# Performance work log

Measured on AMD Instinct MI355X. Metric: run time of the kernel, lower is better.

The kernel has to match this reference:

```python
import jax, jax.numpy as jnp
import numpy as np

N_HEADS = 16
WINDOW = 128
EPS = 1e-6
NEG_INF = -1e30  # effectively -inf after softmax in fp32


def setup_inputs() -> dict:
    key = jax.random.key(0)
    ks = jax.random.split(key, 5)
    B, T, D = 2, 2048, 1024
    scale = 1.0 / np.sqrt(D)
    return {
        "x": jax.random.normal(ks[0], (B, T, D), dtype=jnp.float32),
        "Wq": jax.random.normal(ks[1], (D, D), dtype=jnp.float32) * scale,
        "Wk": jax.random.normal(ks[2], (D, D), dtype=jnp.float32) * scale,
        "Wv": jax.random.normal(ks[3], (D, D), dtype=jnp.float32) * scale,
        "Wo": jax.random.normal(ks[4], (D, D), dtype=jnp.float32) * scale,
    }


def _l2norm(t):
    # torch F.normalize: t / max(||t||, eps)
    n = jnp.sqrt(jnp.sum(t * t, axis=-1, keepdims=True))
    return t / jnp.maximum(n, EPS)


def reference(x, Wq, Wk, Wv, Wo):
    B, T, D = x.shape
    H, hd = N_HEADS, D // N_HEADS
    # projections (torch Linear: x @ W.T), split heads -> [B, H, T, hd]
    def proj(W):
        return jnp.einsum('btd,ed->bte', x, W).reshape(B, T, H, hd).transpose(0, 2, 1, 3)
    q = _l2norm(proj(Wq))
    k = _l2norm(proj(Wk))
    v = proj(Wv)
    # scores [B, H, T, T] (no 1/sqrt(d) scale in the source)
    attn = jnp.einsum('bhqd,bhkd->bhqk', q, k)
    pos = jnp.arange(T)
    rel = pos[None, :] - pos[:, None]            # rel[i, j] = j - i
    mask = (rel < 0) | (rel >= WINDOW)           # allowed: 0 <= j-i < window
    base = jnp.linspace(0.0, 1.0, H, dtype=x.dtype)
    slopes = jnp.power(jnp.asarray(2.0, x.dtype), -(8.0 * base))  # [H]
    alibi = -jnp.abs(rel).astype(x.dtype)[None, :, :] * slopes[:, None, None]  # [H,T,T]
    bias = jnp.where(mask[None, :, :], jnp.asarray(NEG_INF, x.dtype), alibi)
    attn = jax.nn.softmax(attn + bias[None], axis=-1)
    out = jnp.einsum('bhqk,bhkd->bhqd', attn, v)
    out = out.transpose(0, 2, 1, 3).reshape(B, T, D)
    return jnp.einsum('btd,ed->bte', out, Wo)
```

## Files before the change

### kernel.cpp

```cpp
#include <hip/hip_runtime.h>
#include <hip/hip_bf16.h>

#define T_SEQ   2048
#define BATCH   2
#define DMODEL  1024
#define NHEADS  16
#define HDIM    64
#define WINDOW  128

typedef __attribute__((ext_vector_type(8))) short bf16x8;
typedef __attribute__((ext_vector_type(4))) float f32x4;

__device__ inline void gld_lds16(const __hip_bfloat16* g, __hip_bfloat16* l) {
    __builtin_amdgcn_global_load_lds(
        (const __attribute__((address_space(1))) unsigned int*)g,
        (__attribute__((address_space(3))) unsigned int*)l, 16, 0, 0);
}

__global__ __launch_bounds__(256) void cvt_kernel(
    const float* __restrict__ x,  const float* __restrict__ Wq,
    const float* __restrict__ Wk, const float* __restrict__ Wv,
    const float* __restrict__ Wo,
    __hip_bfloat16* __restrict__ xb, __hip_bfloat16* __restrict__ Wb)
{
    const int lid = blockIdx.x;
    const float* src;
    __hip_bfloat16* dst;
    int blk;
    if (lid < 2048) { src = x; dst = xb; blk = lid; }
    else {
        int slot = (lid - 2048) >> 9;
        blk = (lid - 2048) & 511;
        src = (slot == 0) ? Wq : (slot == 1) ? Wk : (slot == 2) ? Wv : Wo;
        dst = Wb + (size_t)slot * 1024 * 1024;
    }
    int i = (blk * 256 + threadIdx.x) * 8;
    float4 a = *(const float4*)(src + i);
    float4 b = *(const float4*)(src + i + 4);
    __hip_bfloat16 pk[8] = {
        __float2bfloat16(a.x), __float2bfloat16(a.y),
        __float2bfloat16(a.z), __float2bfloat16(a.w),
        __float2bfloat16(b.x), __float2bfloat16(b.y),
        __float2bfloat16(b.z), __float2bfloat16(b.w)};
    *(uint4*)(dst + i) = *(uint4*)pk;
}

__global__ __launch_bounds__(256) void gemm_qkv(
    const __hip_bfloat16* __restrict__ A,
    const __hip_bfloat16* __restrict__ W0,
    const __hip_bfloat16* __restrict__ W1,
    const __hip_bfloat16* __restrict__ W2,
    __hip_bfloat16* __restrict__ C0,
    __hip_bfloat16* __restrict__ C1,
    __hip_bfloat16* __restrict__ C2,
    int M, int N, int K)
{
    const int lid   = blockIdx.x + 8 * blockIdx.y + 256 * blockIdx.z;
    const int xcd   = lid & 7;
    const int s     = lid >> 3;
    const int m_loc = s & 7;
    const int rest  = s >> 3;
    const int n_loc = rest & 3;
    const int z     = rest >> 2;

    const __hip_bfloat16* W = (z == 0) ? W0 : (z == 1 ? W1 : W2);
    __hip_bfloat16* C = (z == 0) ? C0 : (z == 1 ? C1 : C2);

    const int m0 = ((xcd & 3) * 8 + m_loc) * 128;
    const int n0 = ((xcd >> 2) * 4 + n_loc) * 128;

    __shared__ __hip_bfloat16 As[128 * 64];
    __shared__ __hip_bfloat16 Bs[128 * 64];

    const int t    = threadIdx.x;
    const int lane = t & 63;
    const int wv   = t >> 6;

    const int drow = lane >> 3;
    const int sl   = lane & 7;

    const int wm   = (wv >> 1) * 64;
    const int wn   = (wv & 1) * 64;
    const int lrow = lane & 15;
    const int quad = lane >> 4;

    f32x4 acc[4][4];
#pragma unroll
    for (int i = 0; i < 4; i++)
#pragma unroll
        for (int j = 0; j < 4; j++)
            acc[i][j] = (f32x4){0.f, 0.f, 0.f, 0.f};

    for (int k0 = 0; k0 < K; k0 += 64) {
#pragma unroll
        for (int inst = 0; inst < 4; inst++) {
            int r0 = wv * 32 + inst * 8;
            int r  = r0 + drow;
            int gcx = (sl - r) & 7;
            gld_lds16(A + (size_t)(m0 + r) * K + k0 + gcx * 8, &As[r0 * 64]);
            gld_lds16(W + (size_t)(n0 + r) * K + k0 + gcx * 8, &Bs[r0 * 64]);
        }
        __syncthreads();

#pragma unroll
        for (int kk = 0; kk < 2; kk++) {
            bf16x8 af[4], bfv[4];
#pragma unroll
            for (int mi = 0; mi < 4; mi++) {
                int r = wm + mi * 16 + lrow;
                af[mi] = *(const bf16x8*)&As[r * 64 + ((kk * 4 + quad + r) & 7) * 8];
            }
#pragma unroll
            for (int ni = 0; ni < 4; ni++) {
                int r = wn + ni * 16 + lrow;
                bfv[ni] = *(const bf16x8*)&Bs[r * 64 + ((kk * 4 + quad + r) & 7) * 8];
            }
#pragma unroll
            for (int mi = 0; mi < 4; mi++)
#pragma unroll
                for (int ni = 0; ni < 4; ni++)
                    acc[mi][ni] = __builtin_amdgcn_mfma_f32_16x16x32_bf16(
                        af[mi], bfv[ni], acc[mi][ni], 0, 0, 0);
        }
        __syncthreads();
    }

    if (z != 2) {
#pragma unroll
        for (int mi = 0; mi < 4; mi++) {
#pragma unroll
            for (int rr = 0; rr < 4; rr++) {
                float ss = 0.f;
#pragma unroll
                for (int ni = 0; ni < 4; ni++)
                    ss += acc[mi][ni][rr] * acc[mi][ni][rr];
                ss += __shfl_xor(ss, 1);
                ss += __shfl_xor(ss, 2);
                ss += __shfl_xor(ss, 4);
                ss += __shfl_xor(ss, 8);
                float inv = 1.0f / fmaxf(sqrtf(ss), 1e-6f);
#pragma unroll
                for (int ni = 0; ni < 4; ni++)
                    acc[mi][ni][rr] *= inv;
            }
        }
    }

#pragma unroll
    for (int mi = 0; mi < 4; mi++) {
#pragma unroll
        for (int rr = 0; rr < 4; rr++) {
            int row = m0 + wm + mi * 16 + quad * 4 + rr;
            __hip_bfloat16* Crow = C + (size_t)row * N + n0 + wn + lrow;
#pragma unroll
            for (int ni = 0; ni < 4; ni++)
                Crow[ni * 16] = __float2bfloat16(acc[mi][ni][rr]);
        }
    }
}

__global__ __launch_bounds__(256) void gemm_o(
    const __hip_bfloat16* __restrict__ A,
    const __hip_bfloat16* __restrict__ W,
    float* __restrict__ C,
    int M, int N, int K)
{
    const int lid   = blockIdx.x + 8 * blockIdx.y;
    const int xcd   = lid & 7;
    const int s     = lid >> 3;
    const int m_loc = s & 15;
    const int n_loc = s >> 4;

    const int m0 = ((xcd & 3) * 16 + m_loc) * 64;
    const int n0 = ((xcd >> 2) * 4 + n_loc) * 128;

    __shared__ __hip_bfloat16 As[64 * 64];
    __shared__ __hip_bfloat16 Bs[128 * 64];

    const int t    = threadIdx.x;
    const int lane = t & 63;
    const int wv   = t >> 6;

    const int drow = lane >> 3;
    const int sl   = lane & 7;

    const int wm   = (wv >> 1) * 32;
    const int wn   = (wv & 1) * 64;
    const int lrow = lane & 15;
    const int quad = lane >> 4;

    f32x4 acc[2][4];
#pragma unroll
    for (int i = 0; i < 2; i++)
#pragma unroll
        for (int j = 0; j < 4; j++)
            acc[i][j] = (f32x4){0.f, 0.f, 0.f, 0.f};

    for (int k0 = 0; k0 < K; k0 += 64) {
#pragma unroll
        for (int inst = 0; inst < 2; inst++) {
            int r0 = wv * 16 + inst * 8;
            int r  = r0 + drow;
            int gcx = (sl - r) & 7;
            gld_lds16(A + (size_t)(m0 + r) * K + k0 + gcx * 8, &As[r0 * 64]);
        }
#pragma unroll
        for (int inst = 0; inst < 4; inst++) {
            int r0 = wv * 32 + inst * 8;
            int r  = r0 + drow;
            int gcx = (sl - r) & 7;
            gld_lds16(W + (size_t)(n0 + r) * K + k0 + gcx * 8, &Bs[r0 * 64]);
        }
        __syncthreads();

#pragma unroll
        for (int kk = 0; kk < 2; kk++) {
            bf16x8 af[2], bfv[4];
#pragma unroll
            for (int mi = 0; mi < 2; mi++) {
                int r = wm + mi * 16 + lrow;
                af[mi] = *(const bf16x8*)&As[r * 64 + ((kk * 4 + quad + r) & 7) * 8];
            }
#pragma unroll
            for (int ni = 0; ni < 4; ni++) {
                int r = wn + ni * 16 + lrow;
                bfv[ni] = *(const bf16x8*)&Bs[r * 64 + ((kk * 4 + quad + r) & 7) * 8];
            }
#pragma unroll
            for (int mi = 0; mi < 2; mi++)
#pragma unroll
                for (int ni = 0; ni < 4; ni++)
                    acc[mi][ni] = __builtin_amdgcn_mfma_f32_16x16x32_bf16(
                        af[mi], bfv[ni], acc[mi][ni], 0, 0, 0);
        }
        __syncthreads();
    }

#pragma unroll
    for (int mi = 0; mi < 2; mi++) {
#pragma unroll
        for (int rr = 0; rr < 4; rr++) {
            int row = m0 + wm + mi * 16 + quad * 4 + rr;
            float* Crow = C + (size_t)row * N + n0 + wn + lrow;
#pragma unroll
            for (int ni = 0; ni < 4; ni++)
                Crow[ni * 16] = acc[mi][ni][rr];
        }
    }
}

__global__ __launch_bounds__(512) void attn_kernel(
    const __hip_bfloat16* __restrict__ Q,
    const __hip_bfloat16* __restrict__ K,
    const __hip_bfloat16* __restrict__ V,
    __hip_bfloat16* __restrict__ O)
{
    const int qb = blockIdx.x * 128;
    const int h  = blockIdx.y;
    const int b  = blockIdx.z;

    __shared__ __hip_bfloat16 KsP[8 * 16 * 168];
    __shared__ __hip_bfloat16 Vt[64 * 264];

    const size_t base = ((size_t)b * T_SEQ) * DMODEL + h * HDIM;
    const int t    = threadIdx.x;
    const int lane = t & 63;
    const int w    = t >> 6;

    {
        const int drow = lane >> 3, sl = lane & 7;
#pragma unroll
        for (int inst = 0; inst < 4; inst++) {
            int r0 = w * 32 + inst * 8;
            int r  = r0 + drow;
            int gcx = (sl - r) & 7;
            int j  = min(qb + r, T_SEQ - 1);
            gld_lds16(K + base + (size_t)j * DMODEL + gcx * 8, &KsP[r0 * 64]);
        }
    }
    if (t < 256) {
        int c  = t & 7;
        int b0 = t >> 3;
        int sg = (b0 & ~7) | ((b0 + c) & 7);
        unsigned short m[8][8];
#pragma unroll
        for (int i = 0; i < 8; i++) {
            int j = min(qb + b0 * 8 + i, T_SEQ - 1);
            uint4 u = *(const uint4*)(V + base + (size_t)j * DMODEL + c * 8);
            unsigned short tmp[8];
            *(uint4*)tmp = u;
#pragma unroll
            for (int e = 0; e < 8; e++) m[e][i] = tmp[e];
        }
#pragma unroll
        for (int e = 0; e < 8; e++)
            *(uint4*)&Vt[(c * 8 + e) * 264 + sg * 8] = *(uint4*)m[e];
    }
    if (t < 64) {
        uint4 zz = {0, 0, 0, 0};
        *(uint4*)&Vt[t * 264 + 256] = zz;
    }
    __syncthreads();

    const int col  = lane & 15;
    const int quad = lane >> 4;
    const float slope = exp2f(-8.0f * (float)h / 15.0f);

    const __hip_bfloat16* qp = Q + base + (size_t)(qb + w * 16 + col) * DMODEL + quad * 8;
    bf16x8 qf0 = *(const bf16x8*)(qp);
    bf16x8 qf1 = *(const bf16x8*)(qp + 32);

    f32x4 sc[9];
#pragma unroll
    for (int kt = 0; kt < 9; kt++) {
        sc[kt] = (f32x4){0.f, 0.f, 0.f, 0.f};
        int r = w * 16 + kt * 16 + col;
        bf16x8 kb0 = *(const bf16x8*)&KsP[r * 64 + ((quad     + r) & 7) * 8];
        bf16x8 kb1 = *(const bf16x8*)&KsP[r * 64 + ((quad + 4 + r) & 7) * 8];
        sc[kt] = __builtin_amdgcn_mfma_f32_16x16x32_bf16(qf0, kb0, sc[kt], 0, 0, 0);
        sc[kt] = __builtin_amdgcn_mfma_f32_16x16x32_bf16(qf1, kb1, sc[kt], 0, 0, 0);
    }

    float mx[4] = {-3e38f, -3e38f, -3e38f, -3e38f};
#pragma unroll
    for (int kt = 0; kt < 9; kt++) {
#pragma unroll
        for (int r = 0; r < 4; r++) {
            int ql  = quad * 4 + r;
            int rel = kt * 16 + col - ql;
            int ka  = qb + w * 16 + kt * 16 + col;
            bool valid = (rel >= 0) && (rel < WINDOW) && (ka < T_SEQ);
            float v = valid ? (sc[kt][r] - (float)rel * slope) : -1e30f;
            sc[kt][r] = v;
            mx[r] = fmaxf(mx[r], v);
        }
    }
#pragma unroll
    for (int r = 0; r < 4; r++) {
        mx[r] = fmaxf(mx[r], __shfl_xor(mx[r], 1));
        mx[r] = fmaxf(mx[r], __shfl_xor(mx[r], 2));
        mx[r] = fmaxf(mx[r], __shfl_xor(mx[r], 4));
        mx[r] = fmaxf(mx[r], __shfl_xor(mx[r], 8));
    }
    float sm[4] = {0.f, 0.f, 0.f, 0.f};
#pragma unroll
    for (int kt = 0; kt < 9; kt++) {
#pragma unroll
        for (int r = 0; r < 4; r++) {
            float e = __expf(sc[kt][r] - mx[r]);
            sc[kt][r] = e;
            sm[r] += e;
        }
    }
#pragma unroll
    for (int r = 0; r < 4; r++) {
        sm[r] += __shfl_xor(sm[r], 1);
        sm[r] += __shfl_xor(sm[r], 2);
        sm[r] += __shfl_xor(sm[r], 4);
        sm[r] += __shfl_xor(sm[r], 8);
        sm[r] = 1.0f / sm[r];
    }

    __syncthreads();
    __hip_bfloat16* Ps = KsP + w * (16 * 168);
#pragma unroll
    for (int kt = 0; kt < 9; kt++)
#pragma unroll
        for (int r = 0; r < 4; r++)
            Ps[(quad * 4 + r) * 168 + kt * 16 + col] = __float2bfloat16(sc[kt][r] * sm[r]);
#pragma unroll
    for (int i = 0; i < 4; i++)
        Ps[(lane & 15) * 168 + 144 + quad * 4 + i] = __float2bfloat16(0.f);
    __syncthreads();

    f32x4 o[4];
#pragma unroll
    for (int nd = 0; nd < 4; nd++) o[nd] = (f32x4){0.f, 0.f, 0.f, 0.f};
#pragma unroll
    for (int kc = 0; kc < 5; kc++) {
        bf16x8 pf = *(const bf16x8*)&Ps[col * 168 + kc * 32 + quad * 8];
        int bblk = w * 2 + kc * 4 + quad;
#pragma unroll
        for (int nd = 0; nd < 4; nd++) {
            int d  = nd * 16 + col;
            int sg = (bblk < 32) ? ((bblk & ~7) | ((bblk + (d >> 3)) & 7)) : 32;
            bf16x8 vf = *(const bf16x8*)&Vt[d * 264 + sg * 8];
            o[nd] = __builtin_amdgcn_mfma_f32_16x16x32_bf16(pf, vf, o[nd], 0, 0, 0);
        }
    }

#pragma unroll
    for (int r = 0; r < 4; r++) {
        __hip_bfloat16* op = O + base + (size_t)(qb + w * 16 + quad * 4 + r) * DMODEL + col;
#pragma unroll
        for (int nd = 0; nd < 4; nd++)
            op[nd * 16] = __float2bfloat16(o[nd][r]);
    }
}

extern "C" void kernel_launch(void* const* d_in, const int* in_sizes, int n_in,
                              void* d_out, int out_size, void* d_ws, size_t ws_size,
                              hipStream_t stream)
{
    const float* x  = (const float*)d_in[0];
    const float* Wq = (const float*)d_in[1];
    const float* Wk = (const float*)d_in[2];
    const float* Wv = (const float*)d_in[3];
    const float* Wo = (const float*)d_in[4];
    float* out = (float*)d_out;

    const size_t MT = (size_t)BATCH * T_SEQ;
    __hip_bfloat16* Qw = (__hip_bfloat16*)d_ws;
    __hip_bfloat16* Kw = Qw + MT * DMODEL;
    __hip_bfloat16* Vw = Kw + MT * DMODEL;
    __hip_bfloat16* XA = Vw + MT * DMODEL;
    __hip_bfloat16* Wb = XA + MT * DMODEL;

    cvt_kernel<<<4096, 256, 0, stream>>>(x, Wq, Wk, Wv, Wo, XA, Wb);

    dim3 g1(DMODEL / 128, MT / 128, 3);
    gemm_qkv<<<g1, 256, 0, stream>>>(
        XA, Wb, Wb + 1024 * 1024, Wb + 2 * 1024 * 1024,
        Qw, Kw, Vw, (int)MT, DMODEL, DMODEL);

    dim3 g2(T_SEQ / 128, NHEADS, BATCH);
    attn_kernel<<<g2, 512, 0, stream>>>(Qw, Kw, Vw, XA);

    dim3 g3(DMODEL / 128, MT / 64, 1);
    gemm_o<<<g3, 256, 0, stream>>>(
        XA, Wb + 3 * 1024 * 1024, out, (int)MT, DMODEL, DMODEL);
}
```

Before: 146.2 us.

## Rewrite QKV GEMM as 256x256 double-buffered ping-pong pipelined kernel

The QKV projection GEMM moves from 128x128 tiles with 256 threads and a single LDS buffer to 256x256 tiles with 512 threads, treating the concatenated Wq/Wk/Wv as one N=3072 matrix. K-tiles are double-buffered, and each stage's global-to-LDS loads are split into quarter-tiles interleaved between MFMA phases, with explicit waitcnt, barriers and setprio. The aim is to hide global load latency behind MFMA work and raise arithmetic intensity per tile. In exchange it uses heavier LDS (128KB), more accumulator registers, and a grid of only 192 blocks on a 256-CU device, so occupancy and load balance are at risk.

```diff
diff --git a/kernel.cpp b/kernel.cpp
--- a/kernel.cpp
+++ b/kernel.cpp
@@ -45,94 +45,208 @@
     *(uint4*)(dst + i) = *(uint4*)pk;
 }
 
-__global__ __launch_bounds__(256) void gemm_qkv(
+__device__ inline void stageA(const __hip_bfloat16* __restrict__ A,
+                              __hip_bfloat16* dst, int m0, int k0, int half,
+                              int w, int lane)
+{
+#pragma unroll
+    for (int i = 0; i < 2; ++i) {
+        int g0   = w * 16 + i * 8;
+        int row0 = (g0 & 63) + ((g0 >> 6) << 7) + (half << 6);
+        int r    = row0 + (lane >> 3);
+        int gcx  = ((lane & 7) - r) & 7;
+        gld_lds16(A + (size_t)(m0 + r) * DMODEL + k0 + gcx * 8, dst + row0 * 64);
+    }
+}
+
+__device__ inline void stageB(const __hip_bfloat16* __restrict__ W,
+                              __hip_bfloat16* dst, int n0, int k0, int half,
+                              int w, int lane)
+{
+#pragma unroll
+    for (int i = 0; i < 2; ++i) {
+        int g0   = w * 16 + i * 8;
+        int row0 = (g0 & 31) + ((g0 >> 5) << 6) + (half << 5);
+        int r    = row0 + (lane >> 3);
+        int gcx  = ((lane & 7) - r) & 7;
+        gld_lds16(W + (size_t)(n0 + r) * DMODEL + k0 + gcx * 8, dst + row0 * 64);
+    }
+}
+
+__device__ inline bf16x8 rdfrag(const __hip_bfloat16* buf, int r, int kc) {
+    return *(const bf16x8*)&buf[r * 64 + (((kc + r) & 7) << 3)];
+}
+
+__global__ __launch_bounds__(512, 2) void gemm_qkv(
     const __hip_bfloat16* __restrict__ A,
-    const __hip_bfloat16* __restrict__ W0,
-    const __hip_bfloat16* __restrict__ W1,
-    const __hip_bfloat16* __restrict__ W2,
+    const __hip_bfloat16* __restrict__ Wp,
     __hip_bfloat16* __restrict__ C0,
     __hip_bfloat16* __restrict__ C1,
-    __hip_bfloat16* __restrict__ C2,
-    int M, int N, int K)
-{
-    const int lid   = blockIdx.x + 8 * blockIdx.y + 256 * blockIdx.z;
-    const int xcd   = lid & 7;
-    const int s     = lid >> 3;
-    const int m_loc = s & 7;
-    const int rest  = s >> 3;
-    const int n_loc = rest & 3;
-    const int z     = rest >> 2;
-
-    const __hip_bfloat16* W = (z == 0) ? W0 : (z == 1 ? W1 : W2);
-    __hip_bfloat16* C = (z == 0) ? C0 : (z == 1 ? C1 : C2);
-
-    const int m0 = ((xcd & 3) * 8 + m_loc) * 128;
-    const int n0 = ((xcd >> 2) * 4 + n_loc) * 128;
-
-    __shared__ __hip_bfloat16 As[128 * 64];
-    __shared__ __hip_bfloat16 Bs[128 * 64];
+    __hip_bfloat16* __restrict__ C2)
+{
+    const int lid   = blockIdx.x;
+    const int wgid  = (lid & 7) * 24 + (lid >> 3);
+    const int bn    = wgid % 12;
+    const int bm    = wgid / 12;
+    const int m0    = bm * 256;
+    const int n0    = bn * 256;
+    const int z     = n0 >> 10;
+    const int cbase = n0 & 1023;
+
+    __shared__ __hip_bfloat16 As[2][256 * 64];
+    __shared__ __hip_bfloat16 Bs[2][256 * 64];
 
     const int t    = threadIdx.x;
     const int lane = t & 63;
-    const int wv   = t >> 6;
-
-    const int drow = lane >> 3;
-    const int sl   = lane & 7;
-
-    const int wm   = (wv >> 1) * 64;
-    const int wn   = (wv & 1) * 64;
+    const int w    = t >> 6;
+    const int wr   = w >> 2;
+    const int wc   = w & 3;
     const int lrow = lane & 15;
     const int quad = lane >> 4;
-
-    f32x4 acc[4][4];
-#pragma unroll
-    for (int i = 0; i < 4; i++)
-#pragma unroll
-        for (int j = 0; j < 4; j++)
+    const int arow = wr * 128;
+    const int brow = wc * 64;
+
+    f32x4 acc[8][4];
+#pragma unroll
+    for (int i = 0; i < 8; ++i)
+#pragma unroll
+        for (int j = 0; j < 4; ++j)
             acc[i][j] = (f32x4){0.f, 0.f, 0.f, 0.f};
 
-    for (int k0 = 0; k0 < K; k0 += 64) {
-#pragma unroll
-        for (int inst = 0; inst < 4; inst++) {
-            int r0 = wv * 32 + inst * 8;
-            int r  = r0 + drow;
-            int gcx = (sl - r) & 7;
-            gld_lds16(A + (size_t)(m0 + r) * K + k0 + gcx * 8, &As[r0 * 64]);
-            gld_lds16(W + (size_t)(n0 + r) * K + k0 + gcx * 8, &Bs[r0 * 64]);
-        }
-        __syncthreads();
-
-#pragma unroll
-        for (int kk = 0; kk < 2; kk++) {
-            bf16x8 af[4], bfv[4];
-#pragma unroll
-            for (int mi = 0; mi < 4; mi++) {
-                int r = wm + mi * 16 + lrow;
-                af[mi] = *(const bf16x8*)&As[r * 64 + ((kk * 4 + quad + r) & 7) * 8];
-            }
-#pragma unroll
-            for (int ni = 0; ni < 4; ni++) {
-                int r = wn + ni * 16 + lrow;
-                bfv[ni] = *(const bf16x8*)&Bs[r * 64 + ((kk * 4 + quad + r) & 7) * 8];
-            }
-#pragma unroll
-            for (int mi = 0; mi < 4; mi++)
-#pragma unroll
-                for (int ni = 0; ni < 4; ni++)
-                    acc[mi][ni] = __builtin_amdgcn_mfma_f32_16x16x32_bf16(
-                        af[mi], bfv[ni], acc[mi][ni], 0, 0, 0);
-        }
-        __syncthreads();
+    stageA(A,  As[0], m0, 0, 0, w, lane);
+    stageB(Wp, Bs[0], n0, 0, 0, w, lane);
+    stageB(Wp, Bs[0], n0, 0, 1, w, lane);
+    stageA(A,  As[0], m0, 0, 1, w, lane);
+    asm volatile("s_waitcnt vmcnt(4)" ::: "memory");
+    __builtin_amdgcn_s_barrier();
+
+    bf16x8 af[4][2];
+    bf16x8 bfr[2][2];
+
+    for (int tt = 0; tt < 16; ++tt) {
+        const int p  = tt & 1;
+        const int pn = p ^ 1;
+        const __hip_bfloat16* Ar = As[p];
+        const __hip_bfloat16* Br = Bs[p];
+        const int k1   = (tt + 1) << 6;
+        const bool pf  = (tt < 15);
+
+#pragma unroll
+        for (int mi = 0; mi < 4; ++mi) {
+            int r = arow + mi * 16 + lrow;
+            af[mi][0] = rdfrag(Ar, r, quad);
+            af[mi][1] = rdfrag(Ar, r, 4 + quad);
+        }
+#pragma unroll
+        for (int ni = 0; ni < 2; ++ni) {
+            int r = brow + ni * 16 + lrow;
+            bfr[ni][0] = rdfrag(Br, r, quad);
+            bfr[ni][1] = rdfrag(Br, r, 4 + quad);
+        }
+        if (pf) stageA(A, As[pn], m0, k1, 0, w, lane);
+        __builtin_amdgcn_s_barrier();
+        asm volatile("s_waitcnt lgkmcnt(0)" ::: "memory");
+        __builtin_amdgcn_sched_barrier(0);
+        __builtin_amdgcn_s_setprio(1);
+#pragma unroll
+        for (int mi = 0; mi < 4; ++mi)
+#pragma unroll
+            for (int ni = 0; ni < 2; ++ni) {
+                acc[mi][ni] = __builtin_amdgcn_mfma_f32_16x16x32_bf16(
+                    af[mi][0], bfr[ni][0], acc[mi][ni], 0, 0, 0);
+                acc[mi][ni] = __builtin_amdgcn_mfma_f32_16x16x32_bf16(
+                    af[mi][1], bfr[ni][1], acc[mi][ni], 0, 0, 0);
+            }
+        __builtin_amdgcn_s_setprio(0);
+        asm volatile("s_waitcnt vmcnt(4)" ::: "memory");
+        __builtin_amdgcn_s_barrier();
+
+#pragma unroll
+        for (int ni = 0; ni < 2; ++ni) {
+            int r = brow + (ni + 2) * 16 + lrow;
+            bfr[ni][0] = rdfrag(Br, r, quad);
+            bfr[ni][1] = rdfrag(Br, r, 4 + quad);
+        }
+        if (pf) stageB(Wp, Bs[pn], n0, k1, 0, w, lane);
+        __builtin_amdgcn_s_barrier();
+        asm volatile("s_waitcnt lgkmcnt(0)" ::: "memory");
+        __builtin_amdgcn_sched_barrier(0);
+        __builtin_amdgcn_s_setprio(1);
+#pragma unroll
+        for (int mi = 0; mi < 4; ++mi)
+#pragma unroll
+            for (int ni = 0; ni < 2; ++ni) {
+                acc[mi][ni + 2] = __builtin_amdgcn_mfma_f32_16x16x32_bf16(
+                    af[mi][0], bfr[ni][0], acc[mi][ni + 2], 0, 0, 0);
+                acc[mi][ni + 2] = __builtin_amdgcn_mfma_f32_16x16x32_bf16(
+                    af[mi][1], bfr[ni][1], acc[mi][ni + 2], 0, 0, 0);
+            }
+        __builtin_amdgcn_s_setprio(0);
+        asm volatile("s_waitcnt vmcnt(4)" ::: "memory");
+        __builtin_amdgcn_s_barrier();
+
+#pragma unroll
+        for (int mi = 0; mi < 4; ++mi) {
+            int r = arow + (mi + 4) * 16 + lrow;
+            af[mi][0] = rdfrag(Ar, r, quad);
+            af[mi][1] = rdfrag(Ar, r, 4 + quad);
+        }
+#pragma unroll
+        for (int ni = 0; ni < 2; ++ni) {
+            int r = brow + ni * 16 + lrow;
+            bfr[ni][0] = rdfrag(Br, r, quad);
+            bfr[ni][1] = rdfrag(Br, r, 4 + quad);
+        }
+        if (pf) stageB(Wp, Bs[pn], n0, k1, 1, w, lane);
+        __builtin_amdgcn_s_barrier();
+        asm volatile("s_waitcnt lgkmcnt(0)" ::: "memory");
+        __builtin_amdgcn_sched_barrier(0);
+        __builtin_amdgcn_s_setprio(1);
+#pragma unroll
+        for (int mi = 0; mi < 4; ++mi)
+#pragma unroll
+            for (int ni = 0; ni < 2; ++ni) {
+                acc[mi + 4][ni] = __builtin_amdgcn_mfma_f32_16x16x32_bf16(
+                    af[mi][0], bfr[ni][0], acc[mi + 4][ni], 0, 0, 0);
+                acc[mi + 4][ni] = __builtin_amdgcn_mfma_f32_16x16x32_bf16(
+                    af[mi][1], bfr[ni][1], acc[mi + 4][ni], 0, 0, 0);
+            }
+        __builtin_amdgcn_s_setprio(0);
+        __builtin_amdgcn_s_barrier();
+
+#pragma unroll
+        for (int ni = 0; ni < 2; ++ni) {
+            int r = brow + (ni + 2) * 16 + lrow;
+            bfr[ni][0] = rdfrag(Br, r, quad);
+            bfr[ni][1] = rdfrag(Br, r, 4 + quad);
+        }
+        if (pf) stageA(A, As[pn], m0, k1, 1, w, lane);
+        __builtin_amdgcn_s_barrier();
+        asm volatile("s_waitcnt lgkmcnt(0)" ::: "memory");
+        __builtin_amdgcn_sched_barrier(0);
+        __builtin_amdgcn_s_setprio(1);
+#pragma unroll
+        for (int mi = 0; mi < 4; ++mi)
+#pragma unroll
+            for (int ni = 0; ni < 2; ++ni) {
+                acc[mi + 4][ni + 2] = __builtin_amdgcn_mfma_f32_16x16x32_bf16(
+                    af[mi][0], bfr[ni][0], acc[mi + 4][ni + 2], 0, 0, 0);
+                acc[mi + 4][ni + 2] = __builtin_amdgcn_mfma_f32_16x16x32_bf16(
+                    af[mi][1], bfr[ni][1], acc[mi + 4][ni + 2], 0, 0, 0);
+            }
+        __builtin_amdgcn_s_setprio(0);
+        asm volatile("s_waitcnt vmcnt(4)" ::: "memory");
+        __builtin_amdgcn_s_barrier();
     }
 
     if (z != 2) {
 #pragma unroll
-        for (int mi = 0; mi < 4; mi++) {
-#pragma unroll
-            for (int rr = 0; rr < 4; rr++) {
+        for (int mi = 0; mi < 8; ++mi) {
+#pragma unroll
+            for (int rr = 0; rr < 4; ++rr) {
                 float ss = 0.f;
 #pragma unroll
-                for (int ni = 0; ni < 4; ni++)
+                for (int ni = 0; ni < 4; ++ni)
                     ss += acc[mi][ni][rr] * acc[mi][ni][rr];
                 ss += __shfl_xor(ss, 1);
                 ss += __shfl_xor(ss, 2);
@@ -140,20 +254,21 @@
                 ss += __shfl_xor(ss, 8);
                 float inv = 1.0f / fmaxf(sqrtf(ss), 1e-6f);
 #pragma unroll
-                for (int ni = 0; ni < 4; ni++)
+                for (int ni = 0; ni < 4; ++ni)
                     acc[mi][ni][rr] *= inv;
             }
         }
     }
 
-#pragma unroll
-    for (int mi = 0; mi < 4; mi++) {
-#pragma unroll
-        for (int rr = 0; rr < 4; rr++) {
-            int row = m0 + wm + mi * 16 + quad * 4 + rr;
-            __hip_bfloat16* Crow = C + (size_t)row * N + n0 + wn + lrow;
-#pragma unroll
-            for (int ni = 0; ni < 4; ni++)
+    __hip_bfloat16* C = (z == 0) ? C0 : (z == 1) ? C1 : C2;
+#pragma unroll
+    for (int mi = 0; mi < 8; ++mi) {
+#pragma unroll
+        for (int rr = 0; rr < 4; ++rr) {
+            int row = m0 + arow + mi * 16 + quad * 4 + rr;
+            __hip_bfloat16* Crow = C + (size_t)row * DMODEL + cbase + brow + lrow;
+#pragma unroll
+            for (int ni = 0; ni < 4; ++ni)
                 Crow[ni * 16] = __float2bfloat16(acc[mi][ni][rr]);
         }
     }
@@ -418,10 +533,7 @@
 
     cvt_kernel<<<4096, 256, 0, stream>>>(x, Wq, Wk, Wv, Wo, XA, Wb);
 
-    dim3 g1(DMODEL / 128, MT / 128, 3);
-    gemm_qkv<<<g1, 256, 0, stream>>>(
-        XA, Wb, Wb + 1024 * 1024, Wb + 2 * 1024 * 1024,
-        Qw, Kw, Vw, (int)MT, DMODEL, DMODEL);
+    gemm_qkv<<<dim3(192), 512, 0, stream>>>(XA, Wb, Qw, Kw, Vw);
 
     dim3 g2(T_SEQ / 128, NHEADS, BATCH);
     attn_kernel<<<g2, 512, 0, stream>>>(Qw, Kw, Vw, XA);
```

After: 157.5 us. +7.7%, slower.

## Pipeline QKV and output GEMMs with 4-stage async LDS ring and larger tiles

Applied to the files above, without the earlier changes.

Both projection GEMMs are rewritten around a 4-slot LDS ring fed three k-steps ahead by global_load_lds. Explicit vmcnt/lgkmcnt waits, a single barrier per step, sched barriers and setprio interleave the MFMAs with the next step's LDS reads. The QKV GEMM becomes one 1D grid of 256x256 tiles with 8 waves over the concatenated weight matrix, and the output GEMM uses 128x128 tiles. The aim is to hide memory latency and cut barrier and launch overhead, at the cost of fewer workgroups (192 and 256), which may underfill the CUs, plus hand-tuned wait counts that are fragile.

```diff
diff --git a/kernel.cpp b/kernel.cpp
--- a/kernel.cpp
+++ b/kernel.cpp
@@ -11,10 +11,23 @@
 typedef __attribute__((ext_vector_type(8))) short bf16x8;
 typedef __attribute__((ext_vector_type(4))) float f32x4;
 
+#define LGKM(n)  asm volatile("s_waitcnt lgkmcnt(" #n ")" ::: "memory")
+#define VMCNT(n) asm volatile("s_waitcnt vmcnt(" #n ")" ::: "memory")
+#define SCHEDB() __builtin_amdgcn_sched_barrier(0)
+#define BAR()    __builtin_amdgcn_s_barrier()
+
 __device__ inline void gld_lds16(const __hip_bfloat16* g, __hip_bfloat16* l) {
     __builtin_amdgcn_global_load_lds(
         (const __attribute__((address_space(1))) unsigned int*)g,
         (__attribute__((address_space(3))) unsigned int*)l, 16, 0, 0);
+}
+
+__device__ inline bf16x8 ds_readb128(const __hip_bfloat16* p) {
+    bf16x8 r;
+    asm volatile("ds_read_b128 %0, %1"
+                 : "=v"(r)
+                 : "v"((const __attribute__((address_space(3))) __hip_bfloat16*)p));
+    return r;
 }
 
 __global__ __launch_bounds__(256) void cvt_kernel(
@@ -45,94 +58,133 @@
     *(uint4*)(dst + i) = *(uint4*)pk;
 }
 
-__global__ __launch_bounds__(256) void gemm_qkv(
+__global__ __launch_bounds__(512, 2) void gemm_qkv(
     const __hip_bfloat16* __restrict__ A,
-    const __hip_bfloat16* __restrict__ W0,
-    const __hip_bfloat16* __restrict__ W1,
-    const __hip_bfloat16* __restrict__ W2,
+    const __hip_bfloat16* __restrict__ Wp,
     __hip_bfloat16* __restrict__ C0,
     __hip_bfloat16* __restrict__ C1,
-    __hip_bfloat16* __restrict__ C2,
-    int M, int N, int K)
+    __hip_bfloat16* __restrict__ C2)
 {
-    const int lid   = blockIdx.x + 8 * blockIdx.y + 256 * blockIdx.z;
-    const int xcd   = lid & 7;
-    const int s     = lid >> 3;
-    const int m_loc = s & 7;
-    const int rest  = s >> 3;
-    const int n_loc = rest & 3;
-    const int z     = rest >> 2;
-
-    const __hip_bfloat16* W = (z == 0) ? W0 : (z == 1 ? W1 : W2);
-    __hip_bfloat16* C = (z == 0) ? C0 : (z == 1 ? C1 : C2);
-
-    const int m0 = ((xcd & 3) * 8 + m_loc) * 128;
-    const int n0 = ((xcd >> 2) * 4 + n_loc) * 128;
-
-    __shared__ __hip_bfloat16 As[128 * 64];
-    __shared__ __hip_bfloat16 Bs[128 * 64];
+    const int lid   = blockIdx.x;
+    const int wgid  = (lid & 7) * 24 + (lid >> 3);
+    const int bn    = wgid % 12;
+    const int bm    = wgid / 12;
+    const int m0    = bm * 256;
+    const int n0    = bn * 256;
+    const int z     = n0 >> 10;
+    const int cbase = n0 & 1023;
+
+    __shared__ __hip_bfloat16 S[4][2][256 * 32];
 
     const int t    = threadIdx.x;
     const int lane = t & 63;
-    const int wv   = t >> 6;
-
-    const int drow = lane >> 3;
-    const int sl   = lane & 7;
-
-    const int wm   = (wv >> 1) * 64;
-    const int wn   = (wv & 1) * 64;
+    const int w    = t >> 6;
+    const int wr   = w >> 2;
+    const int wc   = w & 3;
     const int lrow = lane & 15;
     const int quad = lane >> 4;
-
-    f32x4 acc[4][4];
-#pragma unroll
-    for (int i = 0; i < 4; i++)
-#pragma unroll
-        for (int j = 0; j < 4; j++)
+    const int arow = wr * 128;
+    const int brow = wc * 64;
+
+    f32x4 acc[8][4];
+#pragma unroll
+    for (int i = 0; i < 8; ++i)
+#pragma unroll
+        for (int j = 0; j < 4; ++j)
             acc[i][j] = (f32x4){0.f, 0.f, 0.f, 0.f};
 
-    for (int k0 = 0; k0 < K; k0 += 64) {
-#pragma unroll
-        for (int inst = 0; inst < 4; inst++) {
-            int r0 = wv * 32 + inst * 8;
-            int r  = r0 + drow;
-            int gcx = (sl - r) & 7;
-            gld_lds16(A + (size_t)(m0 + r) * K + k0 + gcx * 8, &As[r0 * 64]);
-            gld_lds16(W + (size_t)(n0 + r) * K + k0 + gcx * 8, &Bs[r0 * 64]);
-        }
-        __syncthreads();
-
-#pragma unroll
-        for (int kk = 0; kk < 2; kk++) {
-            bf16x8 af[4], bfv[4];
-#pragma unroll
-            for (int mi = 0; mi < 4; mi++) {
-                int r = wm + mi * 16 + lrow;
-                af[mi] = *(const bf16x8*)&As[r * 64 + ((kk * 4 + quad + r) & 7) * 8];
-            }
-#pragma unroll
-            for (int ni = 0; ni < 4; ni++) {
-                int r = wn + ni * 16 + lrow;
-                bfv[ni] = *(const bf16x8*)&Bs[r * 64 + ((kk * 4 + quad + r) & 7) * 8];
-            }
-#pragma unroll
-            for (int mi = 0; mi < 4; mi++)
-#pragma unroll
-                for (int ni = 0; ni < 4; ni++)
-                    acc[mi][ni] = __builtin_amdgcn_mfma_f32_16x16x32_bf16(
-                        af[mi], bfv[ni], acc[mi][ni], 0, 0, 0);
-        }
-        __syncthreads();
-    }
+    auto STAGE = [&](int h) {
+        const int slot = h & 3;
+        const int k0   = h * 32;
+        const int r    = (lane >> 2);
+        const int c    = lane & 3;
+#pragma unroll
+        for (int i = 0; i < 2; ++i) {
+            int row0 = i * 128 + w * 16;
+            int row  = row0 + r;
+            int gcx  = (c - row) & 3;
+            gld_lds16(A + (size_t)(m0 + row) * DMODEL + k0 + gcx * 8,
+                      &S[slot][0][row0 * 32]);
+        }
+#pragma unroll
+        for (int i = 0; i < 2; ++i) {
+            int row0 = i * 128 + w * 16;
+            int row  = row0 + r;
+            int gcx  = (c - row) & 3;
+            gld_lds16(Wp + (size_t)(n0 + row) * DMODEL + k0 + gcx * 8,
+                      &S[slot][1][row0 * 32]);
+        }
+    };
+
+    auto RD = [&](const __hip_bfloat16* base, int r) -> bf16x8 {
+        return ds_readb128(base + r * 32 + (((quad + r) & 3) << 3));
+    };
+
+    bf16x8 bf_[2][4], al_[2][4], ah_[2][4];
+
+#define READS_BL(P, H) { \
+    const __hip_bfloat16* Sb = &S[(H) & 3][1][0]; \
+    const __hip_bfloat16* Sa = &S[(H) & 3][0][0]; \
+    _Pragma("unroll") for (int ni = 0; ni < 4; ++ni) \
+        bf_[P][ni] = RD(Sb, brow + ni * 16 + lrow); \
+    _Pragma("unroll") for (int mi = 0; mi < 4; ++mi) \
+        al_[P][mi] = RD(Sa, arow + mi * 16 + lrow); }
+
+#define READS_AH(P, H) { \
+    const __hip_bfloat16* Sa = &S[(H) & 3][0][0]; \
+    _Pragma("unroll") for (int mi = 0; mi < 4; ++mi) \
+        ah_[P][mi] = RD(Sa, arow + 64 + mi * 16 + lrow); }
+
+#define MFMA_L(P) { \
+    _Pragma("unroll") for (int mi = 0; mi < 4; ++mi) \
+    _Pragma("unroll") for (int ni = 0; ni < 4; ++ni) \
+        acc[mi][ni] = __builtin_amdgcn_mfma_f32_16x16x32_bf16( \
+            al_[P][mi], bf_[P][ni], acc[mi][ni], 0, 0, 0); }
+
+#define MFMA_H(P) { \
+    _Pragma("unroll") for (int mi = 0; mi < 4; ++mi) \
+    _Pragma("unroll") for (int ni = 0; ni < 4; ++ni) \
+        acc[mi + 4][ni] = __builtin_amdgcn_mfma_f32_16x16x32_bf16( \
+            ah_[P][mi], bf_[P][ni], acc[mi + 4][ni], 0, 0, 0); }
+
+#define QBODY(H, P, PN, DO_STAGE, DO_READS, MIDGATE) { \
+    if (DO_STAGE) STAGE((H) + 3); \
+    LGKM(4); SCHEDB(); \
+    __builtin_amdgcn_s_setprio(1); MFMA_L(P); __builtin_amdgcn_s_setprio(0); \
+    if (DO_READS) READS_BL(PN, (H) + 1); \
+    MIDGATE; SCHEDB(); \
+    __builtin_amdgcn_s_setprio(1); MFMA_H(P); __builtin_amdgcn_s_setprio(0); \
+    if (DO_READS) READS_AH(PN, (H) + 1); \
+    VMCNT(4); BAR(); }
+
+    STAGE(0); STAGE(1); STAGE(2);
+    VMCNT(4);
+    BAR();
+    READS_BL(0, 0);
+    READS_AH(0, 0);
+
+    for (int it = 0; it < 15; ++it) {
+        const int h = it * 2;
+        QBODY(h,     0, 1, true,        true, LGKM(8));
+        QBODY(h + 1, 1, 0, (it < 14),   true, LGKM(8));
+    }
+    QBODY(30, 0, 1, false, true,  LGKM(8));
+    QBODY(31, 1, 0, false, false, LGKM(0));
+
+#undef QBODY
+#undef MFMA_H
+#undef MFMA_L
+#undef READS_AH
+#undef READS_BL
 
     if (z != 2) {
 #pragma unroll
-        for (int mi = 0; mi < 4; mi++) {
-#pragma unroll
-            for (int rr = 0; rr < 4; rr++) {
+        for (int mi = 0; mi < 8; ++mi) {
+#pragma unroll
+            for (int rr = 0; rr < 4; ++rr) {
                 float ss = 0.f;
 #pragma unroll
-                for (int ni = 0; ni < 4; ni++)
+                for (int ni = 0; ni < 4; ++ni)
                     ss += acc[mi][ni][rr] * acc[mi][ni][rr];
                 ss += __shfl_xor(ss, 1);
                 ss += __shfl_xor(ss, 2);
@@ -140,110 +192,128 @@
                 ss += __shfl_xor(ss, 8);
                 float inv = 1.0f / fmaxf(sqrtf(ss), 1e-6f);
 #pragma unroll
-                for (int ni = 0; ni < 4; ni++)
+                for (int ni = 0; ni < 4; ++ni)
                     acc[mi][ni][rr] *= inv;
             }
         }
     }
 
-#pragma unroll
-    for (int mi = 0; mi < 4; mi++) {
-#pragma unroll
-        for (int rr = 0; rr < 4; rr++) {
-            int row = m0 + wm + mi * 16 + quad * 4 + rr;
-            __hip_bfloat16* Crow = C + (size_t)row * N + n0 + wn + lrow;
-#pragma unroll
-            for (int ni = 0; ni < 4; ni++)
+    __hip_bfloat16* C = (z == 0) ? C0 : (z == 1) ? C1 : C2;
+#pragma unroll
+    for (int mi = 0; mi < 8; ++mi) {
+#pragma unroll
+        for (int rr = 0; rr < 4; ++rr) {
+            int row = m0 + arow + mi * 16 + quad * 4 + rr;
+            __hip_bfloat16* Crow = C + (size_t)row * DMODEL + cbase + brow + lrow;
+#pragma unroll
+            for (int ni = 0; ni < 4; ++ni)
                 Crow[ni * 16] = __float2bfloat16(acc[mi][ni][rr]);
         }
     }
 }
 
-__global__ __launch_bounds__(256) void gemm_o(
+__global__ __launch_bounds__(256, 2) void gemm_o(
     const __hip_bfloat16* __restrict__ A,
     const __hip_bfloat16* __restrict__ W,
-    float* __restrict__ C,
-    int M, int N, int K)
+    float* __restrict__ C)
 {
-    const int lid   = blockIdx.x + 8 * blockIdx.y;
-    const int xcd   = lid & 7;
-    const int s     = lid >> 3;
-    const int m_loc = s & 15;
-    const int n_loc = s >> 4;
-
-    const int m0 = ((xcd & 3) * 16 + m_loc) * 64;
-    const int n0 = ((xcd >> 2) * 4 + n_loc) * 128;
-
-    __shared__ __hip_bfloat16 As[64 * 64];
-    __shared__ __hip_bfloat16 Bs[128 * 64];
+    const int lid  = blockIdx.x;
+    const int wgid = (lid & 7) * 32 + (lid >> 3);
+    const int bn   = wgid & 7;
+    const int bm   = wgid >> 3;
+    const int m0   = bm * 128;
+    const int n0   = bn * 128;
+
+    __shared__ __hip_bfloat16 S[4][2][128 * 32];
 
     const int t    = threadIdx.x;
     const int lane = t & 63;
     const int wv   = t >> 6;
-
-    const int drow = lane >> 3;
-    const int sl   = lane & 7;
-
-    const int wm   = (wv >> 1) * 32;
-    const int wn   = (wv & 1) * 64;
     const int lrow = lane & 15;
     const int quad = lane >> 4;
-
-    f32x4 acc[2][4];
-#pragma unroll
-    for (int i = 0; i < 2; i++)
-#pragma unroll
-        for (int j = 0; j < 4; j++)
+    const int wm   = (wv >> 1) * 64;
+    const int wn   = (wv & 1) * 64;
+
+    f32x4 acc[4][4];
+#pragma unroll
+    for (int i = 0; i < 4; ++i)
+#pragma unroll
+        for (int j = 0; j < 4; ++j)
             acc[i][j] = (f32x4){0.f, 0.f, 0.f, 0.f};
 
-    for (int k0 = 0; k0 < K; k0 += 64) {
-#pragma unroll
-        for (int inst = 0; inst < 2; inst++) {
-            int r0 = wv * 16 + inst * 8;
-            int r  = r0 + drow;
-            int gcx = (sl - r) & 7;
-            gld_lds16(A + (size_t)(m0 + r) * K + k0 + gcx * 8, &As[r0 * 64]);
-        }
-#pragma unroll
-        for (int inst = 0; inst < 4; inst++) {
-            int r0 = wv * 32 + inst * 8;
-            int r  = r0 + drow;
-            int gcx = (sl - r) & 7;
-            gld_lds16(W + (size_t)(n0 + r) * K + k0 + gcx * 8, &Bs[r0 * 64]);
-        }
-        __syncthreads();
-
-#pragma unroll
-        for (int kk = 0; kk < 2; kk++) {
-            bf16x8 af[2], bfv[4];
-#pragma unroll
-            for (int mi = 0; mi < 2; mi++) {
-                int r = wm + mi * 16 + lrow;
-                af[mi] = *(const bf16x8*)&As[r * 64 + ((kk * 4 + quad + r) & 7) * 8];
-            }
-#pragma unroll
-            for (int ni = 0; ni < 4; ni++) {
-                int r = wn + ni * 16 + lrow;
-                bfv[ni] = *(const bf16x8*)&Bs[r * 64 + ((kk * 4 + quad + r) & 7) * 8];
-            }
-#pragma unroll
-            for (int mi = 0; mi < 2; mi++)
-#pragma unroll
-                for (int ni = 0; ni < 4; ni++)
-                    acc[mi][ni] = __builtin_amdgcn_mfma_f32_16x16x32_bf16(
-                        af[mi], bfv[ni], acc[mi][ni], 0, 0, 0);
-        }
-        __syncthreads();
-    }
-
-#pragma unroll
-    for (int mi = 0; mi < 2; mi++) {
-#pragma unroll
-        for (int rr = 0; rr < 4; rr++) {
+    auto STAGE = [&](int h) {
+        const int slot = h & 3;
+        const int k0   = h * 32;
+        const int r    = (lane >> 2);
+        const int c    = lane & 3;
+#pragma unroll
+        for (int i = 0; i < 2; ++i) {
+            int row0 = i * 64 + wv * 16;
+            int row  = row0 + r;
+            int gcx  = (c - row) & 3;
+            gld_lds16(A + (size_t)(m0 + row) * DMODEL + k0 + gcx * 8,
+                      &S[slot][0][row0 * 32]);
+        }
+#pragma unroll
+        for (int i = 0; i < 2; ++i) {
+            int row0 = i * 64 + wv * 16;
+            int row  = row0 + r;
+            int gcx  = (c - row) & 3;
+            gld_lds16(W + (size_t)(n0 + row) * DMODEL + k0 + gcx * 8,
+                      &S[slot][1][row0 * 32]);
+        }
+    };
+
+    auto RD = [&](const __hip_bfloat16* base, int r) -> bf16x8 {
+        return ds_readb128(base + r * 32 + (((quad + r) & 3) << 3));
+    };
+
+    bf16x8 a_[2][4], b_[2][4];
+
+#define READS_O(P, H) { \
+    const __hip_bfloat16* Sa = &S[(H) & 3][0][0]; \
+    const __hip_bfloat16* Sb = &S[(H) & 3][1][0]; \
+    _Pragma("unroll") for (int mi = 0; mi < 4; ++mi) \
+        a_[P][mi] = RD(Sa, wm + mi * 16 + lrow); \
+    _Pragma("unroll") for (int ni = 0; ni < 4; ++ni) \
+        b_[P][ni] = RD(Sb, wn + ni * 16 + lrow); }
+
+#define OBODY(H, P, PN, DO_STAGE, DO_READS, GATE) { \
+    if (DO_STAGE) STAGE((H) + 3); \
+    if (DO_READS) READS_O(PN, (H) + 1); \
+    GATE; SCHEDB(); \
+    __builtin_amdgcn_s_setprio(1); \
+    _Pragma("unroll") for (int mi = 0; mi < 4; ++mi) \
+    _Pragma("unroll") for (int ni = 0; ni < 4; ++ni) \
+        acc[mi][ni] = __builtin_amdgcn_mfma_f32_16x16x32_bf16( \
+            a_[P][mi], b_[P][ni], acc[mi][ni], 0, 0, 0); \
+    __builtin_amdgcn_s_setprio(0); \
+    VMCNT(4); BAR(); }
+
+    STAGE(0); STAGE(1); STAGE(2);
+    VMCNT(4);
+    BAR();
+    READS_O(0, 0);
+
+    for (int it = 0; it < 15; ++it) {
+        const int h = it * 2;
+        OBODY(h,     0, 1, true,      true, LGKM(8));
+        OBODY(h + 1, 1, 0, (it < 14), true, LGKM(8));
+    }
+    OBODY(30, 0, 1, false, true,  LGKM(8));
+    OBODY(31, 1, 0, false, false, LGKM(0));
+
+#undef OBODY
+#undef READS_O
+
+#pragma unroll
+    for (int mi = 0; mi < 4; ++mi) {
+#pragma unroll
+        for (int rr = 0; rr < 4; ++rr) {
             int row = m0 + wm + mi * 16 + quad * 4 + rr;
-            float* Crow = C + (size_t)row * N + n0 + wn + lrow;
-#pragma unroll
-            for (int ni = 0; ni < 4; ni++)
+            float* Crow = C + (size_t)row * DMODEL + n0 + wn + lrow;
+#pragma unroll
+            for (int ni = 0; ni < 4; ++ni)
                 Crow[ni * 16] = acc[mi][ni][rr];
         }
     }
@@ -418,15 +488,10 @@
 
     cvt_kernel<<<4096, 256, 0, stream>>>(x, Wq, Wk, Wv, Wo, XA, Wb);
 
-    dim3 g1(DMODEL / 128, MT / 128, 3);
-    gemm_qkv<<<g1, 256, 0, stream>>>(
-        XA, Wb, Wb + 1024 * 1024, Wb + 2 * 1024 * 1024,
-        Qw, Kw, Vw, (int)MT, DMODEL, DMODEL);
+    gemm_qkv<<<dim3(192), 512, 0, stream>>>(XA, Wb, Qw, Kw, Vw);
 
     dim3 g2(T_SEQ / 128, NHEADS, BATCH);
     attn_kernel<<<g2, 512, 0, stream>>>(Qw, Kw, Vw, XA);
 
-    dim3 g3(DMODEL / 128, MT / 64, 1);
-    gemm_o<<<g3, 256, 0, stream>>>(
-        XA, Wb + 3 * 1024 * 1024, out, (int)MT, DMODEL, DMODEL);
-}
+    gemm_o<<<dim3(256), 256, 0, stream>>>(XA, Wb + 3 * 1024 * 1024, out);
+}
```

Result: no change. 148.5 us (+1.6%).
